# Performance work log

Hardware: AMD Instinct MI355X
Metric: run time of the kernel (lower is better)

## Reference

```python
import jax, jax.numpy as jnp
import numpy as np

VS, EMB, HS, B, T = 128, 64, 512, 256, 512

def setup_inputs() -> dict:
    key = jax.random.key(0)
    ks = jax.random.split(key, 12)
    s = lambda k, shape, fan: jax.random.normal(k, shape, jnp.float32) / np.sqrt(fan)
    return {
        "x": jax.random.randint(ks[0], (B, T), 0, VS),
        "embedding": s(ks[1], (VS, EMB), EMB),
        "W_ih0": s(ks[2], (EMB, HS), EMB), "b_ih0": jnp.zeros((HS,), jnp.float32),
        "W_hh0": s(ks[3], (HS, HS), HS),   "b_hh0": jnp.zeros((HS,), jnp.float32),
        "W_ih1": s(ks[4], (HS, HS), HS),   "b_ih1": jnp.zeros((HS,), jnp.float32),
        "W_hh1": s(ks[5], (HS, HS), HS),   "b_hh1": jnp.zeros((HS,), jnp.float32),
        "W_fc": s(ks[6], (HS, VS), HS),    "b_fc": jnp.zeros((VS,), jnp.float32),
    }

def _rnn(x, embedding, W_ih0, b_ih0, W_hh0, b_hh0, W_ih1, b_ih1, W_hh1, b_hh1, W_fc, b_fc):
    emb = embedding[x]                     # [B, T, EMB]
    emb_t = jnp.swapaxes(emb, 0, 1)        # [T, B, EMB]
    Bsz = x.shape[0]
    h0 = jnp.zeros((Bsz, W_hh0.shape[0]), embedding.dtype)
    h1 = jnp.zeros((Bsz, W_hh1.shape[0]), embedding.dtype)

    def step(carry, inp):
        h0, h1 = carry
        h0 = jnp.tanh(inp @ W_ih0 + b_ih0 + h0 @ W_hh0 + b_hh0)
        h1 = jnp.tanh(h0 @ W_ih1 + b_ih1 + h1 @ W_hh1 + b_hh1)
        return (h0, h1), h1

    (h0, h1), outs = jax.lax.scan(step, (h0, h1), emb_t)   # outs: [T, B, HS]
    out = jnp.swapaxes(outs, 0, 1)                          # [B, T, HS]
    logits = out @ W_fc + b_fc                              # [B, T, VS]
    return logits, (h0, h1)

def reference(x, embedding, W_ih0, b_ih0, W_hh0, b_hh0, W_ih1, b_ih1, W_hh1, b_hh1, W_fc, b_fc):
    logits, hidden = _rnn(x, embedding, W_ih0, b_ih0, W_hh0, b_hh0,
                          W_ih1, b_ih1, W_hh1, b_hh1, W_fc, b_fc)
    return logits
```

## Files before the change

### kernel.cpp

```cpp
#include <hip/hip_runtime.h>
#include <hip/hip_bf16.h>

#define VSZ 128
#define EMBD 64
#define HSZ 512
#define BSZ 256
#define TLEN 512
#define NBLK 136

typedef __attribute__((ext_vector_type(8))) short short8;
typedef __attribute__((ext_vector_type(4))) float f32x4;
typedef __attribute__((ext_vector_type(4))) unsigned int u32x4;
typedef __hip_bfloat16 bf16;

#define SQ   ((size_t)HSZ*HSZ)

#define O_WHH0HI ((size_t)0)
#define O_WHH0LO (O_WHH0HI + SQ)
#define O_WIH1HI (O_WHH0LO + SQ)
#define O_WIH1LO (O_WIH1HI + SQ)
#define O_WHH1HI (O_WIH1LO + SQ)
#define O_WHH1LO (O_WHH1HI + SQ)
#define O_WIH0HI (O_WHH1LO + SQ)
#define O_WIH0LO (O_WIH0HI + (size_t)HSZ*EMBD)
#define O_WFCHI  (O_WIH0LO + (size_t)HSZ*EMBD)
#define O_WFCLO  (O_WFCHI + (size_t)VSZ*HSZ)
#define O_EMBHI  (O_WFCLO + (size_t)VSZ*HSZ)
#define O_EMBLO  (O_EMBHI + (size_t)VSZ*EMBD)

#define O_RINGB  ((size_t)3571712)
#define RGRING   (3*8192)
#define O_H0R_B  (O_RINGB)
#define O_H1R_B  (O_RINGB + (size_t)16*RGRING*4)
#define O_CTR_B  (O_H1R_B + (size_t)16*RGRING*4)
#define CTRN     224

#define ASTR   1024
#define SMEMSZ 65536

static __device__ __forceinline__ short8 ld8(const bf16* p) { return *(const short8*)p; }
static __device__ __forceinline__ float b2f(bf16 v) { return __bfloat162float(v); }
#define MFMA(a,b,c) __builtin_amdgcn_mfma_f32_16x16x32_bf16((a),(b),(c),0,0,0)

static __device__ __forceinline__ void st4_sc(void* p, unsigned v) {
    asm volatile("global_store_dword %0, %1, off sc0 sc1" :: "v"(p), "v"(v) : "memory");
}
static __device__ __forceinline__ void st4i(int* p, int v) { st4_sc(p, (unsigned)v); }
static __device__ __forceinline__ void pref4sc(const unsigned* base, int tid, u32x4* v) {
    const unsigned* p0 = base + 0*2048 + tid*4;
    const unsigned* p1 = base + 1*2048 + tid*4;
    const unsigned* p2 = base + 2*2048 + tid*4;
    const unsigned* p3 = base + 3*2048 + tid*4;
    asm volatile(
        "global_load_dwordx4 %0, %4, off sc0 sc1\n\t"
        "global_load_dwordx4 %1, %5, off sc0 sc1\n\t"
        "global_load_dwordx4 %2, %6, off sc0 sc1\n\t"
        "global_load_dwordx4 %3, %7, off sc0 sc1\n\t"
        "s_waitcnt vmcnt(0)"
        : "=&v"(v[0]), "=&v"(v[1]), "=&v"(v[2]), "=&v"(v[3])
        : "v"(p0), "v"(p1), "v"(p2), "v"(p3) : "memory");
}
static __device__ __forceinline__ void pref8sc(const unsigned* b1, const unsigned* b2,
                                               int tid, u32x4* v) {
    const unsigned* q0 = b1 + 0*2048 + tid*4; const unsigned* q1 = b1 + 1*2048 + tid*4;
    const unsigned* q2 = b1 + 2*2048 + tid*4; const unsigned* q3 = b1 + 3*2048 + tid*4;
    const unsigned* q4 = b2 + 0*2048 + tid*4; const unsigned* q5 = b2 + 1*2048 + tid*4;
    const unsigned* q6 = b2 + 2*2048 + tid*4; const unsigned* q7 = b2 + 3*2048 + tid*4;
    asm volatile(
        "global_load_dwordx4 %0, %8, off sc0 sc1\n\t"
        "global_load_dwordx4 %1, %9, off sc0 sc1\n\t"
        "global_load_dwordx4 %2, %10, off sc0 sc1\n\t"
        "global_load_dwordx4 %3, %11, off sc0 sc1\n\t"
        "global_load_dwordx4 %4, %12, off sc0 sc1\n\t"
        "global_load_dwordx4 %5, %13, off sc0 sc1\n\t"
        "global_load_dwordx4 %6, %14, off sc0 sc1\n\t"
        "global_load_dwordx4 %7, %15, off sc0 sc1\n\t"
        "s_waitcnt vmcnt(0)"
        : "=&v"(v[0]), "=&v"(v[1]), "=&v"(v[2]), "=&v"(v[3]),
          "=&v"(v[4]), "=&v"(v[5]), "=&v"(v[6]), "=&v"(v[7])
        : "v"(q0), "v"(q1), "v"(q2), "v"(q3), "v"(q4), "v"(q5), "v"(q6), "v"(q7)
        : "memory");
}
static __device__ __forceinline__ void ld3x16sc(const unsigned* p0, const unsigned* p1,
                                                const unsigned* p2, u32x4* v) {
    asm volatile(
        "global_load_dwordx4 %0, %3, off sc0 sc1\n\t"
        "global_load_dwordx4 %1, %4, off sc0 sc1\n\t"
        "global_load_dwordx4 %2, %5, off sc0 sc1\n\t"
        "s_waitcnt vmcnt(0)"
        : "=&v"(v[0]), "=&v"(v[1]), "=&v"(v[2])
        : "v"(p0), "v"(p1), "v"(p2) : "memory");
}
static __device__ __forceinline__ void pollv(const int* p, int need, bool act, int wv) {
    if (wv == 0) {
        for (int it = 0; it < (1 << 17); ++it) {
            int ok = 1;
            if (act) {
                int v;
                asm volatile("global_load_dword %0, %1, off sc0 sc1\n\t"
                             "s_waitcnt vmcnt(0)" : "=v"(v) : "v"(p) : "memory");
                ok = (v >= need);
            }
            if (__all(ok)) break;
            __builtin_amdgcn_s_sleep(2);
        }
    }
    __syncthreads();
}
static __device__ __forceinline__ void awriteQ(char* Ahi, char* Alo, int tid,
                                               u32x4 v, int rowoff, int kbase) {
    int row = rowoff + (tid >> 5);
    int colb = kbase * 2 + (tid & 31) * 8;
    int off = row * ASTR + (colb ^ ((row & 7) << 4));
    uint2 hi, lo;
    hi.x = (v[0] & 0xffffu) | (v[1] << 16);  hi.y = (v[2] & 0xffffu) | (v[3] << 16);
    lo.x = (v[0] >> 16) | (v[1] & 0xffff0000u); lo.y = (v[2] >> 16) | (v[3] & 0xffff0000u);
    *(uint2*)(Ahi + off) = hi;
    *(uint2*)(Alo + off) = lo;
}

__global__ void k_prep(const float* __restrict__ emb, const float* __restrict__ Wih0,
                       const float* __restrict__ Whh0, const float* __restrict__ Wih1,
                       const float* __restrict__ Whh1, const float* __restrict__ Wfc,
                       bf16* __restrict__ ws) {
    int j = blockIdx.x * blockDim.x + threadIdx.x;
    const int SQi = HSZ * HSZ;
    if (j < SQi) {
        int n = j / HSZ, k = j - n * HSZ;
        float w = Whh0[k * HSZ + n];
        bf16 hi = __float2bfloat16(w);
        ws[O_WHH0HI + j] = hi; ws[O_WHH0LO + j] = __float2bfloat16(w - b2f(hi));
        return;
    }
    j -= SQi;
    if (j < SQi) {
        int n = j / HSZ, k = j - n * HSZ;
        float w = Wih1[k * HSZ + n];
        bf16 hi = __float2bfloat16(w);
        ws[O_WIH1HI + j] = hi; ws[O_WIH1LO + j] = __float2bfloat16(w - b2f(hi));
        return;
    }
    j -= SQi;
    if (j < SQi) {
        int n = j / HSZ, k = j - n * HSZ;
        float w = Whh1[k * HSZ + n];
        bf16 hi = __float2bfloat16(w);
        ws[O_WHH1HI + j] = hi; ws[O_WHH1LO + j] = __float2bfloat16(w - b2f(hi));
        return;
    }
    j -= SQi;
    if (j < HSZ * EMBD) {
        int n = j / EMBD, k = j - n * EMBD;
        float w = Wih0[k * HSZ + n];
        bf16 hi = __float2bfloat16(w);
        ws[O_WIH0HI + j] = hi; ws[O_WIH0LO + j] = __float2bfloat16(w - b2f(hi));
        return;
    }
    j -= HSZ * EMBD;
    if (j < VSZ * HSZ) {
        int n = j / HSZ, k = j - n * HSZ;
        float w = Wfc[k * VSZ + n];
        bf16 hi = __float2bfloat16(w);
        ws[O_WFCHI + j] = hi; ws[O_WFCLO + j] = __float2bfloat16(w - b2f(hi));
        return;
    }
    j -= VSZ * HSZ;
    if (j < VSZ * EMBD) {
        float w = emb[j];
        bf16 hi = __float2bfloat16(w);
        ws[O_EMBHI + j] = hi; ws[O_EMBLO + j] = __float2bfloat16(w - b2f(hi));
        return;
    }
    j -= VSZ * EMBD;
    if (j < CTRN * 64) ((int*)((char*)ws + O_CTR_B))[j] = 0;
}

__global__ __launch_bounds__(512, 1) void k_persist(
    const int* __restrict__ x,
    const float* __restrict__ bih0, const float* __restrict__ bhh0,
    const float* __restrict__ bih1, const float* __restrict__ bhh1,
    const float* __restrict__ bfc,
    bf16* __restrict__ ws, float* __restrict__ out)
{
    extern __shared__ char smem[];
    const int tid = (int)threadIdx.x;
    const int lane = tid & 63;
    const int wv   = tid >> 6;
    const int l15  = lane & 15;
    const int quad = lane >> 4;
    const int bid  = (int)blockIdx.x;
    const int swz  = (l15 & 7) << 4;

    int* CTR = (int*)((char*)ws + O_CTR_B);
#define XPROD(rg,qq) (CTR + (size_t)((rg)*4+(qq))*64)
#define YPROD(rg,qq) (CTR + (size_t)(64+(rg)*4+(qq))*64)
#define YCONS(rg,qq) (CTR + (size_t)(136+(rg)*4+(qq))*64)
#define FCC(f)       (CTR + (size_t)(200+(f))*64)
#define H0R(rg) ((unsigned*)((char*)ws + O_H0R_B) + (size_t)(rg)*RGRING)
#define H1R(rg) ((unsigned*)((char*)ws + O_H1R_B) + (size_t)(rg)*RGRING)

    if (bid < 64) {
        const int rg = bid >> 2, q = bid & 3, mb = rg * 16, qb = q * 128;
        char* Ahi = smem;
        char* Alo = smem + 16384;
        char* Ehi = smem + 32768;
        char* Elo = smem + 34816;
        const bf16* embhi = ws + O_EMBHI; const bf16* emblo = ws + O_EMBLO;
        const int col = qb + wv * 16 + l15;
        const float bias = bih0[col] + bhh0[col];
        const bf16* wch = ws + O_WHH0HI + (size_t)col * HSZ + quad * 8;
        const bf16* wcl = ws + O_WHH0LO + (size_t)col * HSZ + quad * 8;
        const bf16* ech = ws + O_WIH0HI + (size_t)col * EMBD + quad * 8;
        const bf16* ecl = ws + O_WIH0LO + (size_t)col * EMBD + quad * 8;
        unsigned* h0r = H0R(rg);
        const int qa = (q + 1) & 3, qb2 = (q + 2) & 3, qc = (q + 3) & 3;

        for (int i = tid * 4; i < 32768; i += 2048) *(unsigned*)(smem + i) = 0u;
        __syncthreads();

        int scur = 0;
        for (int t = 0; t < TLEN; ++t) {
            const int sp = (scur == 0) ? 2 : scur - 1;
            const int* pp = nullptr; int nd = 0; bool act = false;
            if (wv == 0) {
                if (lane < 3) {
                    int ss = (lane == 0) ? qa : (lane == 1) ? qb2 : qc;
                    pp = XPROD(rg, ss); nd = t; act = (t > 0);
                } else if (lane < 7) {
                    pp = YCONS(rg, lane - 3); nd = t - 2; act = (t >= 3);
                }
            }
            pollv(pp, nd, act, wv);
            if (t > 0) {
                const unsigned* sl = h0r + (size_t)sp * 8192;
                u32x4 v3[3];
                ld3x16sc(sl + qa*2048 + tid*4, sl + qb2*2048 + tid*4, sl + qc*2048 + tid*4, v3);
                awriteQ(Ahi, Alo, tid, v3[0], 0, qa * 128);
                awriteQ(Ahi, Alo, tid, v3[1], 0, qb2 * 128);
                awriteQ(Ahi, Alo, tid, v3[2], 0, qc * 128);
            }
            if (tid < 128) {
                int row = tid >> 3, oct = tid & 7;
                int xr = x[(size_t)(mb + row) * TLEN + t];
                int eoff = row * 128 + ((oct * 16) ^ ((row & 7) << 4));
                *(short8*)(Ehi + eoff) = ld8(embhi + (size_t)xr * EMBD + oct * 8);
                *(short8*)(Elo + eoff) = ld8(emblo + (size_t)xr * EMBD + oct * 8);
            }
            __syncthreads();
            f32x4 accA = {}, accB = {};
#pragma unroll
            for (int kc = 0; kc < 2; kc++) {
                int aoff = l15 * 128 + ((kc * 64 + quad * 16) ^ swz);
                short8 ah = *(const short8*)(Ehi + aoff);
                short8 al = *(const short8*)(Elo + aoff);
                short8 bh = ld8(ech + kc * 32);
                short8 bl = ld8(ecl + kc * 32);
                accA = MFMA(ah, bh, accA); accB = MFMA(al, bh, accB); accB = MFMA(ah, bl, accB);
            }
#pragma unroll
            for (int kc = 0; kc < 16; kc++) {
                int aoff = l15 * ASTR + ((kc * 64 + quad * 16) ^ swz);
                short8 ah = *(const short8*)(Ahi + aoff);
                short8 al = *(const short8*)(Alo + aoff);
                short8 bh = ld8(wch + kc * 32);
                short8 bl = ld8(wcl + kc * 32);
                accA = MFMA(ah, bh, accA); accB = MFMA(al, bh, accB); accB = MFMA(ah, bl, accB);
            }
            __syncthreads();
            unsigned* slot = h0r + (size_t)scur * 8192 + q * 2048;
#pragma unroll
            for (int rr = 0; rr < 4; rr++) {
                int row = quad * 4 + rr;
                float v = tanhf(accA[rr] + accB[rr] + bias);
                bf16 hb = __float2bfloat16(v);
                bf16 lb = __float2bfloat16(v - b2f(hb));
                unsigned short hu, lu;
                __builtin_memcpy(&hu, &hb, 2); __builtin_memcpy(&lu, &lb, 2);
                int loff = row * ASTR + ((col * 2) ^ ((row & 7) << 4));
                *(unsigned short*)(Ahi + loff) = hu;
                *(unsigned short*)(Alo + loff) = lu;
                st4_sc(slot + (size_t)row * 128 + wv * 16 + l15,
                       (unsigned)hu | ((unsigned)lu << 16));
            }
            asm volatile("s_waitcnt vmcnt(0)" ::: "memory");
            __syncthreads();
            if (tid == 0) st4i(XPROD(rg, q), t + 1);
            scur = (scur == 2) ? 0 : scur + 1;
        }

    } else if (bid < 128) {
        const int rg = (bid - 64) >> 2, q = (bid - 64) & 3, qb = q * 128;
        char* A1hi = smem;
        char* A1lo = smem + 16384;
        char* A2hi = smem + 32768;
        char* A2lo = smem + 49152;
        const int col = qb + wv * 16 + l15;
        const float bias = bih1[col] + bhh1[col];
        const bf16* whh = ws + O_WHH1HI + (size_t)col * HSZ + quad * 8;
        const bf16* whl = ws + O_WHH1LO + (size_t)col * HSZ + quad * 8;
        const bf16* w1h = ws + O_WIH1HI + (size_t)col * HSZ + quad * 8;
        const bf16* w1l = ws + O_WIH1LO + (size_t)col * HSZ + quad * 8;
        unsigned* h1r = H1R(rg);
        const unsigned* h0r = H0R(rg);
        const int qa = (q + 1) & 3, qb2 = (q + 2) & 3, qc = (q + 3) & 3;
        const int f = rg >> 1;

        for (int i = tid * 4; i < 32768; i += 2048) *(unsigned*)(smem + i) = 0u;
        __syncthreads();

        int scur = 0;
        for (int t = 0; t < TLEN; ++t) {
            const int sp = (scur == 0) ? 2 : scur - 1;
            const int* pp = nullptr; int nd = 0; bool act = false;
            if (wv == 0) {
                if (lane < 3) {
                    int ss = (lane == 0) ? qa : (lane == 1) ? qb2 : qc;
                    pp = YPROD(rg, ss); nd = t; act = (t > 0);
                } else if (lane == 3) { pp = FCC(f); nd = t - 2; act = (t >= 3); }
            }
            pollv(pp, nd, act, wv);
            if (t > 0) {
                const unsigned* sl = h1r + (size_t)sp * 8192;
                u32x4 v3[3];
                ld3x16sc(sl + qa*2048 + tid*4, sl + qb2*2048 + tid*4, sl + qc*2048 + tid*4, v3);
                awriteQ(A1hi, A1lo, tid, v3[0], 0, qa * 128);
                awriteQ(A1hi, A1lo, tid, v3[1], 0, qb2 * 128);
                awriteQ(A1hi, A1lo, tid, v3[2], 0, qc * 128);
            }
            __syncthreads();
            f32x4 accA = {}, accB = {};
#pragma unroll
            for (int kc = 0; kc < 16; kc++) {
                int aoff = l15 * ASTR + ((kc * 64 + quad * 16) ^ swz);
                short8 ah = *(const short8*)(A1hi + aoff);
                short8 al = *(const short8*)(A1lo + aoff);
                short8 bh = ld8(whh + kc * 32);
                short8 bl = ld8(whl + kc * 32);
                accA = MFMA(ah, bh, accA); accB = MFMA(al, bh, accB); accB = MFMA(ah, bl, accB);
            }
            pp = nullptr; nd = 0; act = false;
            if (wv == 0 && lane < 4) { pp = XPROD(rg, lane); nd = t + 1; act = true; }
            pollv(pp, nd, act, wv);
            u32x4 pf[4];
            pref4sc(h0r + (size_t)scur * 8192, tid, pf);
#pragma unroll
            for (int c = 0; c < 4; c++) awriteQ(A2hi, A2lo, tid, pf[c], 0, c * 128);
            __syncthreads();
            if (tid == 0) st4i(YCONS(rg, q), t + 1);
#pragma unroll
            for (int kc = 0; kc < 16; kc++) {
                int aoff = l15 * ASTR + ((kc * 64 + quad * 16) ^ swz);
                short8 ah = *(const short8*)(A2hi + aoff);
                short8 al = *(const short8*)(A2lo + aoff);
                short8 bh = ld8(w1h + kc * 32);
                short8 bl = ld8(w1l + kc * 32);
                accA = MFMA(ah, bh, accA); accB = MFMA(al, bh, accB); accB = MFMA(ah, bl, accB);
            }
            __syncthreads();
            unsigned* slot = h1r + (size_t)scur * 8192 + q * 2048;
#pragma unroll
            for (int rr = 0; rr < 4; rr++) {
                int row = quad * 4 + rr;
                float v = tanhf(accA[rr] + accB[rr] + bias);
                bf16 hb = __float2bfloat16(v);
                bf16 lb = __float2bfloat16(v - b2f(hb));
                unsigned short hu, lu;
                __builtin_memcpy(&hu, &hb, 2); __builtin_memcpy(&lu, &lb, 2);
                int loff = row * ASTR + ((col * 2) ^ ((row & 7) << 4));
                *(unsigned short*)(A1hi + loff) = hu;
                *(unsigned short*)(A1lo + loff) = lu;
                st4_sc(slot + (size_t)row * 128 + wv * 16 + l15,
                       (unsigned)hu | ((unsigned)lu << 16));
            }
            asm volatile("s_waitcnt vmcnt(0)" ::: "memory");
            __syncthreads();
            if (tid == 0) st4i(YPROD(rg, q), t + 1);
            scur = (scur == 2) ? 0 : scur + 1;
        }

    } else {
        const int f = bid - 128;
        char* FAhi = smem;
        char* FAlo = smem + 32768;
        const int col = wv * 16 + l15;
        const float bias = bfc[col];
        const bf16* wfh = ws + O_WFCHI + (size_t)col * HSZ + quad * 8;
        const bf16* wfl = ws + O_WFCLO + (size_t)col * HSZ + quad * 8;
        const unsigned* r1 = H1R(2 * f);
        const unsigned* r2 = H1R(2 * f + 1);

        int scur = 0;
        for (int t = 0; t < TLEN; ++t) {
            const int* pp = nullptr; int nd = 0; bool act = false;
            if (wv == 0 && lane < 8) {
                pp = YPROD(2 * f + (lane >> 2), lane & 3); nd = t + 1; act = true;
            }
            pollv(pp, nd, act, wv);
            u32x4 pf[8];
            pref8sc(r1 + (size_t)scur * 8192, r2 + (size_t)scur * 8192, tid, pf);
#pragma unroll
            for (int i = 0; i < 8; i++)
                awriteQ(FAhi, FAlo, tid, pf[i], (i >> 2) * 16, (i & 3) * 128);
            __syncthreads();
            if (tid == 0) st4i(FCC(f), t + 1);
            f32x4 accA[2] = {}, accB[2] = {};
#pragma unroll
            for (int kc = 0; kc < 16; kc++) {
                short8 bh = ld8(wfh + kc * 32);
                short8 bl = ld8(wfl + kc * 32);
#pragma unroll
                for (int mi = 0; mi < 2; mi++) {
                    int aoff = (mi * 16 + l15) * ASTR + ((kc * 64 + quad * 16) ^ swz);
                    short8 ah = *(const short8*)(FAhi + aoff);
                    short8 al = *(const short8*)(FAlo + aoff);
                    accA[mi] = MFMA(ah, bh, accA[mi]);
                    accB[mi] = MFMA(al, bh, accB[mi]);
                    accB[mi] = MFMA(ah, bl, accB[mi]);
                }
            }
#pragma unroll
            for (int mi = 0; mi < 2; mi++)
#pragma unroll
                for (int rr = 0; rr < 4; rr++) {
                    int row = 32 * f + mi * 16 + quad * 4 + rr;
                    out[((size_t)row * TLEN + t) * VSZ + col] = accA[mi][rr] + accB[mi][rr] + bias;
                }
            scur = (scur == 2) ? 0 : scur + 1;
        }
    }
#undef XPROD
#undef YPROD
#undef YCONS
#undef FCC
#undef H0R
#undef H1R
}

extern "C" void kernel_launch(void* const* d_in, const int* in_sizes, int n_in,
                              void* d_out, int out_size, void* d_ws, size_t ws_size,
                              hipStream_t stream) {
    const int*   x    = (const int*)d_in[0];
    const float* emb  = (const float*)d_in[1];
    const float* Wih0 = (const float*)d_in[2];
    const float* bih0 = (const float*)d_in[3];
    const float* Whh0 = (const float*)d_in[4];
    const float* bhh0 = (const float*)d_in[5];
    const float* Wih1 = (const float*)d_in[6];
    const float* bih1 = (const float*)d_in[7];
    const float* Whh1 = (const float*)d_in[8];
    const float* bhh1 = (const float*)d_in[9];
    const float* Wfc  = (const float*)d_in[10];
    const float* bfc  = (const float*)d_in[11];
    float* out = (float*)d_out;
    bf16* ws   = (bf16*)d_ws;

    const int total = 3 * HSZ * HSZ + HSZ * EMBD + VSZ * HSZ + VSZ * EMBD + CTRN * 64;
    k_prep<<<(total + 255) / 256, 256, 0, stream>>>(emb, Wih0, Whh0, Wih1, Whh1, Wfc, ws);

    k_persist<<<NBLK, 512, SMEMSZ, stream>>>(x, bih0, bhh0, bih1, bhh1, bfc, ws, out);
}
```

Baseline: 9.039 ms.

## Merge layer-1 poll and loads into single sync point per timestep

```diff
diff --git a/kernel.cpp b/kernel.cpp
--- a/kernel.cpp
+++ b/kernel.cpp
@@ -91,6 +91,24 @@
         : "=&v"(v[0]), "=&v"(v[1]), "=&v"(v[2])
         : "v"(p0), "v"(p1), "v"(p2) : "memory");
 }
+static __device__ __forceinline__ void ld7x16sc(
+    const unsigned* p0, const unsigned* p1, const unsigned* p2,
+    const unsigned* p3, const unsigned* p4, const unsigned* p5, const unsigned* p6,
+    u32x4* v) {
+    asm volatile(
+        "global_load_dwordx4 %0, %7, off sc0 sc1\n\t"
+        "global_load_dwordx4 %1, %8, off sc0 sc1\n\t"
+        "global_load_dwordx4 %2, %9, off sc0 sc1\n\t"
+        "global_load_dwordx4 %3, %10, off sc0 sc1\n\t"
+        "global_load_dwordx4 %4, %11, off sc0 sc1\n\t"
+        "global_load_dwordx4 %5, %12, off sc0 sc1\n\t"
+        "global_load_dwordx4 %6, %13, off sc0 sc1\n\t"
+        "s_waitcnt vmcnt(0)"
+        : "=&v"(v[0]), "=&v"(v[1]), "=&v"(v[2]), "=&v"(v[3]),
+          "=&v"(v[4]), "=&v"(v[5]), "=&v"(v[6])
+        : "v"(p0), "v"(p1), "v"(p2), "v"(p3), "v"(p4), "v"(p5), "v"(p6)
+        : "memory");
+}
 static __device__ __forceinline__ void pollv(const int* p, int need, bool act, int wv) {
     if (wv == 0) {
         for (int it = 0; it < (1 << 17); ++it) {
@@ -102,7 +120,7 @@
                 ok = (v >= need);
             }
             if (__all(ok)) break;
-            __builtin_amdgcn_s_sleep(2);
+            __builtin_amdgcn_s_sleep(1);
         }
     }
     __syncthreads();
@@ -317,17 +335,29 @@
                     int ss = (lane == 0) ? qa : (lane == 1) ? qb2 : qc;
                     pp = YPROD(rg, ss); nd = t; act = (t > 0);
                 } else if (lane == 3) { pp = FCC(f); nd = t - 2; act = (t >= 3); }
+                else if (lane < 8)    { pp = XPROD(rg, lane - 4); nd = t + 1; act = true; }
             }
             pollv(pp, nd, act, wv);
+            const unsigned* h0s = h0r + (size_t)scur * 8192;
             if (t > 0) {
                 const unsigned* sl = h1r + (size_t)sp * 8192;
-                u32x4 v3[3];
-                ld3x16sc(sl + qa*2048 + tid*4, sl + qb2*2048 + tid*4, sl + qc*2048 + tid*4, v3);
-                awriteQ(A1hi, A1lo, tid, v3[0], 0, qa * 128);
-                awriteQ(A1hi, A1lo, tid, v3[1], 0, qb2 * 128);
-                awriteQ(A1hi, A1lo, tid, v3[2], 0, qc * 128);
-            }
-            __syncthreads();
+                u32x4 v7[7];
+                ld7x16sc(sl + qa*2048 + tid*4, sl + qb2*2048 + tid*4, sl + qc*2048 + tid*4,
+                         h0s + 0*2048 + tid*4, h0s + 1*2048 + tid*4,
+                         h0s + 2*2048 + tid*4, h0s + 3*2048 + tid*4, v7);
+                awriteQ(A1hi, A1lo, tid, v7[0], 0, qa * 128);
+                awriteQ(A1hi, A1lo, tid, v7[1], 0, qb2 * 128);
+                awriteQ(A1hi, A1lo, tid, v7[2], 0, qc * 128);
+#pragma unroll
+                for (int c = 0; c < 4; c++) awriteQ(A2hi, A2lo, tid, v7[3 + c], 0, c * 128);
+            } else {
+                u32x4 pf[4];
+                pref4sc(h0s, tid, pf);
+#pragma unroll
+                for (int c = 0; c < 4; c++) awriteQ(A2hi, A2lo, tid, pf[c], 0, c * 128);
+            }
+            __syncthreads();
+            if (tid == 0) st4i(YCONS(rg, q), t + 1);
             f32x4 accA = {}, accB = {};
 #pragma unroll
             for (int kc = 0; kc < 16; kc++) {
@@ -338,15 +368,6 @@
                 short8 bl = ld8(whl + kc * 32);
                 accA = MFMA(ah, bh, accA); accB = MFMA(al, bh, accB); accB = MFMA(ah, bl, accB);
             }
-            pp = nullptr; nd = 0; act = false;
-            if (wv == 0 && lane < 4) { pp = XPROD(rg, lane); nd = t + 1; act = true; }
-            pollv(pp, nd, act, wv);
-            u32x4 pf[4];
-            pref4sc(h0r + (size_t)scur * 8192, tid, pf);
-#pragma unroll
-            for (int c = 0; c < 4; c++) awriteQ(A2hi, A2lo, tid, pf[c], 0, c * 128);
-            __syncthreads();
-            if (tid == 0) st4i(YCONS(rg, q), t + 1);
 #pragma unroll
             for (int kc = 0; kc < 16; kc++) {
                 int aoff = l15 * ASTR + ((kc * 64 + quad * 16) ^ swz);
```

Result: faster. 8.791 ms (-2.7%).

## Merge layer-0 and layer-1 RNN blocks into one block per row-group slice

Applied to the files above, without the earlier changes.

```diff
diff --git a/kernel.cpp b/kernel.cpp
--- a/kernel.cpp
+++ b/kernel.cpp
@@ -6,7 +6,7 @@
 #define HSZ 512
 #define BSZ 256
 #define TLEN 512
-#define NBLK 136
+#define NBLK 72
 
 typedef __attribute__((ext_vector_type(8))) short short8;
 typedef __attribute__((ext_vector_type(4))) float f32x4;
@@ -46,19 +46,15 @@
     asm volatile("global_store_dword %0, %1, off sc0 sc1" :: "v"(p), "v"(v) : "memory");
 }
 static __device__ __forceinline__ void st4i(int* p, int v) { st4_sc(p, (unsigned)v); }
-static __device__ __forceinline__ void pref4sc(const unsigned* base, int tid, u32x4* v) {
-    const unsigned* p0 = base + 0*2048 + tid*4;
-    const unsigned* p1 = base + 1*2048 + tid*4;
-    const unsigned* p2 = base + 2*2048 + tid*4;
-    const unsigned* p3 = base + 3*2048 + tid*4;
+static __device__ __forceinline__ void ld3x16sc(const unsigned* p0, const unsigned* p1,
+                                                const unsigned* p2, u32x4* v) {
     asm volatile(
-        "global_load_dwordx4 %0, %4, off sc0 sc1\n\t"
-        "global_load_dwordx4 %1, %5, off sc0 sc1\n\t"
-        "global_load_dwordx4 %2, %6, off sc0 sc1\n\t"
-        "global_load_dwordx4 %3, %7, off sc0 sc1\n\t"
+        "global_load_dwordx4 %0, %3, off sc0 sc1\n\t"
+        "global_load_dwordx4 %1, %4, off sc0 sc1\n\t"
+        "global_load_dwordx4 %2, %5, off sc0 sc1\n\t"
         "s_waitcnt vmcnt(0)"
-        : "=&v"(v[0]), "=&v"(v[1]), "=&v"(v[2]), "=&v"(v[3])
-        : "v"(p0), "v"(p1), "v"(p2), "v"(p3) : "memory");
+        : "=&v"(v[0]), "=&v"(v[1]), "=&v"(v[2])
+        : "v"(p0), "v"(p1), "v"(p2) : "memory");
 }
 static __device__ __forceinline__ void pref8sc(const unsigned* b1, const unsigned* b2,
                                                int tid, u32x4* v) {
@@ -81,16 +77,6 @@
         : "v"(q0), "v"(q1), "v"(q2), "v"(q3), "v"(q4), "v"(q5), "v"(q6), "v"(q7)
         : "memory");
 }
-static __device__ __forceinline__ void ld3x16sc(const unsigned* p0, const unsigned* p1,
-                                                const unsigned* p2, u32x4* v) {
-    asm volatile(
-        "global_load_dwordx4 %0, %3, off sc0 sc1\n\t"
-        "global_load_dwordx4 %1, %4, off sc0 sc1\n\t"
-        "global_load_dwordx4 %2, %5, off sc0 sc1\n\t"
-        "s_waitcnt vmcnt(0)"
-        : "=&v"(v[0]), "=&v"(v[1]), "=&v"(v[2])
-        : "v"(p0), "v"(p1), "v"(p2) : "memory");
-}
 static __device__ __forceinline__ void pollv(const int* p, int need, bool act, int wv) {
     if (wv == 0) {
         for (int it = 0; it < (1 << 17); ++it) {
@@ -102,7 +88,7 @@
                 ok = (v >= need);
             }
             if (__all(ok)) break;
-            __builtin_amdgcn_s_sleep(2);
+            __builtin_amdgcn_s_sleep(1);
         }
     }
     __syncthreads();
@@ -192,143 +178,116 @@
     const int swz  = (l15 & 7) << 4;
 
     int* CTR = (int*)((char*)ws + O_CTR_B);
-#define XPROD(rg,qq) (CTR + (size_t)((rg)*4+(qq))*64)
-#define YPROD(rg,qq) (CTR + (size_t)(64+(rg)*4+(qq))*64)
-#define YCONS(rg,qq) (CTR + (size_t)(136+(rg)*4+(qq))*64)
-#define FCC(f)       (CTR + (size_t)(200+(f))*64)
+#define HP0(i)  (CTR + (size_t)(i) * 64)
+#define HPR(i)  (CTR + (size_t)(64 + (i)) * 64)
+#define FCC(f)  (CTR + (size_t)(128 + (f)) * 64)
 #define H0R(rg) ((unsigned*)((char*)ws + O_H0R_B) + (size_t)(rg)*RGRING)
 #define H1R(rg) ((unsigned*)((char*)ws + O_H1R_B) + (size_t)(rg)*RGRING)
 
     if (bid < 64) {
-        const int rg = bid >> 2, q = bid & 3, mb = rg * 16, qb = q * 128;
-        char* Ahi = smem;
-        char* Alo = smem + 16384;
-        char* Ehi = smem + 32768;
-        char* Elo = smem + 34816;
+        const int rg = bid >> 2, q = bid & 3, mb = rg * 16, qcb = q * 128;
+        char* A0hi = smem;
+        char* A0lo = smem + 16384;
+        char* A1hi = smem + 32768;
+        char* A1lo = smem + 49152;
         const bf16* embhi = ws + O_EMBHI; const bf16* emblo = ws + O_EMBLO;
-        const int col = qb + wv * 16 + l15;
-        const float bias = bih0[col] + bhh0[col];
-        const bf16* wch = ws + O_WHH0HI + (size_t)col * HSZ + quad * 8;
-        const bf16* wcl = ws + O_WHH0LO + (size_t)col * HSZ + quad * 8;
-        const bf16* ech = ws + O_WIH0HI + (size_t)col * EMBD + quad * 8;
-        const bf16* ecl = ws + O_WIH0LO + (size_t)col * EMBD + quad * 8;
+        const int col = qcb + wv * 16 + l15;
+        const float b0 = bih0[col] + bhh0[col];
+        const float b1 = bih1[col] + bhh1[col];
+        const bf16* w0h = ws + O_WHH0HI + (size_t)col * HSZ + quad * 8;
+        const bf16* w0l = ws + O_WHH0LO + (size_t)col * HSZ + quad * 8;
+        const bf16* e0h = ws + O_WIH0HI + (size_t)col * EMBD + quad * 8;
+        const bf16* e0l = ws + O_WIH0LO + (size_t)col * EMBD + quad * 8;
+        const bf16* w1h = ws + O_WIH1HI + (size_t)col * HSZ + quad * 8;
+        const bf16* w1l = ws + O_WIH1LO + (size_t)col * HSZ + quad * 8;
+        const bf16* whh = ws + O_WHH1HI + (size_t)col * HSZ + quad * 8;
+        const bf16* whl = ws + O_WHH1LO + (size_t)col * HSZ + quad * 8;
         unsigned* h0r = H0R(rg);
+        unsigned* h1r = H1R(rg);
         const int qa = (q + 1) & 3, qb2 = (q + 2) & 3, qc = (q + 3) & 3;
-
-        for (int i = tid * 4; i < 32768; i += 2048) *(unsigned*)(smem + i) = 0u;
+        const int f = rg >> 1;
+        const int sib0 = rg * 4 + qa, sib1 = rg * 4 + qb2, sib2 = rg * 4 + qc;
+
+        for (int i = tid * 4; i < 65536; i += 2048) *(unsigned*)(smem + i) = 0u;
         __syncthreads();
 
-        int scur = 0;
         for (int t = 0; t < TLEN; ++t) {
-            const int sp = (scur == 0) ? 2 : scur - 1;
+            const int sc_ = t % 3;
+            const int sp_ = (t + 2) % 3;
             const int* pp = nullptr; int nd = 0; bool act = false;
             if (wv == 0) {
-                if (lane < 3) {
-                    int ss = (lane == 0) ? qa : (lane == 1) ? qb2 : qc;
-                    pp = XPROD(rg, ss); nd = t; act = (t > 0);
-                } else if (lane < 7) {
-                    pp = YCONS(rg, lane - 3); nd = t - 2; act = (t >= 3);
-                }
+                if (lane == 0)      { pp = HPR(sib0); nd = t; act = (t > 0); }
+                else if (lane == 1) { pp = HPR(sib1); nd = t; act = (t > 0); }
+                else if (lane == 2) { pp = HPR(sib2); nd = t; act = (t > 0); }
+                else if (lane == 3) { pp = FCC(f);    nd = t - 2; act = (t >= 3); }
             }
             pollv(pp, nd, act, wv);
             if (t > 0) {
-                const unsigned* sl = h0r + (size_t)sp * 8192;
+                const unsigned* sl = h1r + (size_t)sp_ * 8192;
                 u32x4 v3[3];
                 ld3x16sc(sl + qa*2048 + tid*4, sl + qb2*2048 + tid*4, sl + qc*2048 + tid*4, v3);
-                awriteQ(Ahi, Alo, tid, v3[0], 0, qa * 128);
-                awriteQ(Ahi, Alo, tid, v3[1], 0, qb2 * 128);
-                awriteQ(Ahi, Alo, tid, v3[2], 0, qc * 128);
-            }
-            if (tid < 128) {
-                int row = tid >> 3, oct = tid & 7;
-                int xr = x[(size_t)(mb + row) * TLEN + t];
-                int eoff = row * 128 + ((oct * 16) ^ ((row & 7) << 4));
-                *(short8*)(Ehi + eoff) = ld8(embhi + (size_t)xr * EMBD + oct * 8);
-                *(short8*)(Elo + eoff) = ld8(emblo + (size_t)xr * EMBD + oct * 8);
-            }
-            __syncthreads();
-            f32x4 accA = {}, accB = {};
-#pragma unroll
-            for (int kc = 0; kc < 2; kc++) {
-                int aoff = l15 * 128 + ((kc * 64 + quad * 16) ^ swz);
-                short8 ah = *(const short8*)(Ehi + aoff);
-                short8 al = *(const short8*)(Elo + aoff);
-                short8 bh = ld8(ech + kc * 32);
-                short8 bl = ld8(ecl + kc * 32);
-                accA = MFMA(ah, bh, accA); accB = MFMA(al, bh, accB); accB = MFMA(ah, bl, accB);
+                awriteQ(A1hi, A1lo, tid, v3[0], 0, qa * 128);
+                awriteQ(A1hi, A1lo, tid, v3[1], 0, qb2 * 128);
+                awriteQ(A1hi, A1lo, tid, v3[2], 0, qc * 128);
+            }
+            const int xr = x[(size_t)(mb + l15) * TLEN + t];
+            short8 eh0 = ld8(embhi + (size_t)xr * EMBD + quad * 8);
+            short8 el0 = ld8(emblo + (size_t)xr * EMBD + quad * 8);
+            short8 eh1 = ld8(embhi + (size_t)xr * EMBD + 32 + quad * 8);
+            short8 el1 = ld8(emblo + (size_t)xr * EMBD + 32 + quad * 8);
+            __syncthreads();
+            f32x4 aA = {}, aB = {};
+            {
+                short8 bh = ld8(e0h), bl = ld8(e0l);
+                aA = MFMA(eh0, bh, aA); aB = MFMA(el0, bh, aB); aB = MFMA(eh0, bl, aB);
+                bh = ld8(e0h + 32); bl = ld8(e0l + 32);
+                aA = MFMA(eh1, bh, aA); aB = MFMA(el1, bh, aB); aB = MFMA(eh1, bl, aB);
             }
 #pragma unroll
             for (int kc = 0; kc < 16; kc++) {
                 int aoff = l15 * ASTR + ((kc * 64 + quad * 16) ^ swz);
-                short8 ah = *(const short8*)(Ahi + aoff);
-                short8 al = *(const short8*)(Alo + aoff);
-                short8 bh = ld8(wch + kc * 32);
-                short8 bl = ld8(wcl + kc * 32);
-                accA = MFMA(ah, bh, accA); accB = MFMA(al, bh, accB); accB = MFMA(ah, bl, accB);
-            }
-            __syncthreads();
-            unsigned* slot = h0r + (size_t)scur * 8192 + q * 2048;
+                short8 ah = *(const short8*)(A0hi + aoff);
+                short8 al = *(const short8*)(A0lo + aoff);
+                short8 bh = ld8(w0h + kc * 32);
+                short8 bl = ld8(w0l + kc * 32);
+                aA = MFMA(ah, bh, aA); aB = MFMA(al, bh, aB); aB = MFMA(ah, bl, aB);
+            }
+            __syncthreads();
+            unsigned* slot0 = h0r + (size_t)sc_ * 8192 + q * 2048;
 #pragma unroll
             for (int rr = 0; rr < 4; rr++) {
                 int row = quad * 4 + rr;
-                float v = tanhf(accA[rr] + accB[rr] + bias);
+                float v = tanhf(aA[rr] + aB[rr] + b0);
                 bf16 hb = __float2bfloat16(v);
                 bf16 lb = __float2bfloat16(v - b2f(hb));
                 unsigned short hu, lu;
                 __builtin_memcpy(&hu, &hb, 2); __builtin_memcpy(&lu, &lb, 2);
                 int loff = row * ASTR + ((col * 2) ^ ((row & 7) << 4));
-                *(unsigned short*)(Ahi + loff) = hu;
-                *(unsigned short*)(Alo + loff) = lu;
-                st4_sc(slot + (size_t)row * 128 + wv * 16 + l15,
+                *(unsigned short*)(A0hi + loff) = hu;
+                *(unsigned short*)(A0lo + loff) = lu;
+                st4_sc(slot0 + (size_t)row * 128 + wv * 16 + l15,
                        (unsigned)hu | ((unsigned)lu << 16));
             }
             asm volatile("s_waitcnt vmcnt(0)" ::: "memory");
             __syncthreads();
-            if (tid == 0) st4i(XPROD(rg, q), t + 1);
-            scur = (scur == 2) ? 0 : scur + 1;
-        }
-
-    } else if (bid < 128) {
-        const int rg = (bid - 64) >> 2, q = (bid - 64) & 3, qb = q * 128;
-        char* A1hi = smem;
-        char* A1lo = smem + 16384;
-        char* A2hi = smem + 32768;
-        char* A2lo = smem + 49152;
-        const int col = qb + wv * 16 + l15;
-        const float bias = bih1[col] + bhh1[col];
-        const bf16* whh = ws + O_WHH1HI + (size_t)col * HSZ + quad * 8;
-        const bf16* whl = ws + O_WHH1LO + (size_t)col * HSZ + quad * 8;
-        const bf16* w1h = ws + O_WIH1HI + (size_t)col * HSZ + quad * 8;
-        const bf16* w1l = ws + O_WIH1LO + (size_t)col * HSZ + quad * 8;
-        unsigned* h1r = H1R(rg);
-        const unsigned* h0r = H0R(rg);
-        const int qa = (q + 1) & 3, qb2 = (q + 2) & 3, qc = (q + 3) & 3;
-        const int f = rg >> 1;
-
-        for (int i = tid * 4; i < 32768; i += 2048) *(unsigned*)(smem + i) = 0u;
-        __syncthreads();
-
-        int scur = 0;
-        for (int t = 0; t < TLEN; ++t) {
-            const int sp = (scur == 0) ? 2 : scur - 1;
-            const int* pp = nullptr; int nd = 0; bool act = false;
+            if (tid == 0) st4i(HP0(rg * 4 + q), t + 1);
+            pp = nullptr; nd = 0; act = false;
             if (wv == 0) {
-                if (lane < 3) {
-                    int ss = (lane == 0) ? qa : (lane == 1) ? qb2 : qc;
-                    pp = YPROD(rg, ss); nd = t; act = (t > 0);
-                } else if (lane == 3) { pp = FCC(f); nd = t - 2; act = (t >= 3); }
+                if (lane == 0)      { pp = HP0(sib0); nd = t + 1; act = true; }
+                else if (lane == 1) { pp = HP0(sib1); nd = t + 1; act = true; }
+                else if (lane == 2) { pp = HP0(sib2); nd = t + 1; act = true; }
             }
             pollv(pp, nd, act, wv);
-            if (t > 0) {
-                const unsigned* sl = h1r + (size_t)sp * 8192;
+            {
+                const unsigned* sl = h0r + (size_t)sc_ * 8192;
                 u32x4 v3[3];
                 ld3x16sc(sl + qa*2048 + tid*4, sl + qb2*2048 + tid*4, sl + qc*2048 + tid*4, v3);
-                awriteQ(A1hi, A1lo, tid, v3[0], 0, qa * 128);
-                awriteQ(A1hi, A1lo, tid, v3[1], 0, qb2 * 128);
-                awriteQ(A1hi, A1lo, tid, v3[2], 0, qc * 128);
-            }
-            __syncthreads();
-            f32x4 accA = {}, accB = {};
+                awriteQ(A0hi, A0lo, tid, v3[0], 0, qa * 128);
+                awriteQ(A0hi, A0lo, tid, v3[1], 0, qb2 * 128);
+                awriteQ(A0hi, A0lo, tid, v3[2], 0, qc * 128);
+            }
+            __syncthreads();
+            f32x4 cA = {}, cB = {};
 #pragma unroll
             for (int kc = 0; kc < 16; kc++) {
                 int aoff = l15 * ASTR + ((kc * 64 + quad * 16) ^ swz);
@@ -336,32 +295,23 @@
                 short8 al = *(const short8*)(A1lo + aoff);
                 short8 bh = ld8(whh + kc * 32);
                 short8 bl = ld8(whl + kc * 32);
-                accA = MFMA(ah, bh, accA); accB = MFMA(al, bh, accB); accB = MFMA(ah, bl, accB);
-            }
-            pp = nullptr; nd = 0; act = false;
-            if (wv == 0 && lane < 4) { pp = XPROD(rg, lane); nd = t + 1; act = true; }
-            pollv(pp, nd, act, wv);
-            u32x4 pf[4];
-            pref4sc(h0r + (size_t)scur * 8192, tid, pf);
-#pragma unroll
-            for (int c = 0; c < 4; c++) awriteQ(A2hi, A2lo, tid, pf[c], 0, c * 128);
-            __syncthreads();
-            if (tid == 0) st4i(YCONS(rg, q), t + 1);
+                cA = MFMA(ah, bh, cA); cB = MFMA(al, bh, cB); cB = MFMA(ah, bl, cB);
+            }
 #pragma unroll
             for (int kc = 0; kc < 16; kc++) {
                 int aoff = l15 * ASTR + ((kc * 64 + quad * 16) ^ swz);
-                short8 ah = *(const short8*)(A2hi + aoff);
-                short8 al = *(const short8*)(A2lo + aoff);
+                short8 ah = *(const short8*)(A0hi + aoff);
+                short8 al = *(const short8*)(A0lo + aoff);
                 short8 bh = ld8(w1h + kc * 32);
                 short8 bl = ld8(w1l + kc * 32);
-                accA = MFMA(ah, bh, accA); accB = MFMA(al, bh, accB); accB = MFMA(ah, bl, accB);
-            }
-            __syncthreads();
-            unsigned* slot = h1r + (size_t)scur * 8192 + q * 2048;
+                cA = MFMA(ah, bh, cA); cB = MFMA(al, bh, cB); cB = MFMA(ah, bl, cB);
+            }
+            __syncthreads();
+            unsigned* slot1 = h1r + (size_t)sc_ * 8192 + q * 2048;
 #pragma unroll
             for (int rr = 0; rr < 4; rr++) {
                 int row = quad * 4 + rr;
-                float v = tanhf(accA[rr] + accB[rr] + bias);
+                float v = tanhf(cA[rr] + cB[rr] + b1);
                 bf16 hb = __float2bfloat16(v);
                 bf16 lb = __float2bfloat16(v - b2f(hb));
                 unsigned short hu, lu;
@@ -369,17 +319,16 @@
                 int loff = row * ASTR + ((col * 2) ^ ((row & 7) << 4));
                 *(unsigned short*)(A1hi + loff) = hu;
                 *(unsigned short*)(A1lo + loff) = lu;
-                st4_sc(slot + (size_t)row * 128 + wv * 16 + l15,
+                st4_sc(slot1 + (size_t)row * 128 + wv * 16 + l15,
                        (unsigned)hu | ((unsigned)lu << 16));
             }
             asm volatile("s_waitcnt vmcnt(0)" ::: "memory");
             __syncthreads();
-            if (tid == 0) st4i(YPROD(rg, q), t + 1);
-            scur = (scur == 2) ? 0 : scur + 1;
+            if (tid == 0) st4i(HPR(rg * 4 + q), t + 1);
         }
 
     } else {
-        const int f = bid - 128;
+        const int f = bid - 64, mb = f * 32;
         char* FAhi = smem;
         char* FAlo = smem + 32768;
         const int col = wv * 16 + l15;
@@ -389,15 +338,15 @@
         const unsigned* r1 = H1R(2 * f);
         const unsigned* r2 = H1R(2 * f + 1);
 
-        int scur = 0;
         for (int t = 0; t < TLEN; ++t) {
+            const int sc_ = t % 3;
             const int* pp = nullptr; int nd = 0; bool act = false;
             if (wv == 0 && lane < 8) {
-                pp = YPROD(2 * f + (lane >> 2), lane & 3); nd = t + 1; act = true;
+                pp = HPR((2 * f + (lane >> 2)) * 4 + (lane & 3)); nd = t + 1; act = true;
             }
             pollv(pp, nd, act, wv);
             u32x4 pf[8];
-            pref8sc(r1 + (size_t)scur * 8192, r2 + (size_t)scur * 8192, tid, pf);
+            pref8sc(r1 + (size_t)sc_ * 8192, r2 + (size_t)sc_ * 8192, tid, pf);
 #pragma unroll
             for (int i = 0; i < 8; i++)
                 awriteQ(FAhi, FAlo, tid, pf[i], (i >> 2) * 16, (i & 3) * 128);
@@ -422,15 +371,13 @@
             for (int mi = 0; mi < 2; mi++)
 #pragma unroll
                 for (int rr = 0; rr < 4; rr++) {
-                    int row = 32 * f + mi * 16 + quad * 4 + rr;
+                    int row = mb + mi * 16 + quad * 4 + rr;
                     out[((size_t)row * TLEN + t) * VSZ + col] = accA[mi][rr] + accB[mi][rr] + bias;
                 }
-            scur = (scur == 2) ? 0 : scur + 1;
         }
     }
-#undef XPROD
-#undef YPROD
-#undef YCONS
+#undef HP0
+#undef HPR
 #undef FCC
 #undef H0R
 #undef H1R
```

Result: slower. 14.06 ms (+55.5%).
